# Kernel optimization log

Hardware: AMD Instinct MI355X
Metric: run time of the kernel (lower is better)

The kernel has to match this reference:

```python
import jax, jax.numpy as jnp
import numpy as np

N = 100000
E = 2000000
IN_DIM = 5
D = 32
L = 3
EPS = 1e-5


def setup_inputs() -> dict:
    key = jax.random.key(0)
    ks = jax.random.split(key, 10)
    x = jax.random.normal(ks[0], (N, IN_DIM), dtype=jnp.float32)
    edge_index = jax.random.randint(ks[1], (2, E), 0, N, dtype=jnp.int64)
    s = 1.0 / np.sqrt(D)
    w_in = jax.random.normal(ks[2], (D, IN_DIM), dtype=jnp.float32) / np.sqrt(IN_DIM)
    b_in = jnp.zeros((D,), dtype=jnp.float32)
    w_l = jax.random.normal(ks[3], (L, D, D), dtype=jnp.float32) * s  # lin_l per layer
    b_l = jnp.zeros((L, D), dtype=jnp.float32)
    w_r = jax.random.normal(ks[4], (L, D, D), dtype=jnp.float32) * s  # lin_r per layer (no bias, as in PyG SAGEConv)
    gamma = jnp.ones((D,), dtype=jnp.float32)
    beta = jnp.zeros((D,), dtype=jnp.float32)
    return {"x": x, "edge_index": edge_index, "w_in": w_in, "b_in": b_in,
            "w_l": w_l, "b_l": b_l, "w_r": w_r, "gamma": gamma, "beta": beta}


def _layernorm(h, gamma, beta):
    mu = jnp.mean(h, axis=-1, keepdims=True)
    var = jnp.mean(jnp.square(h - mu), axis=-1, keepdims=True)
    return (h - mu) * jax.lax.rsqrt(var + EPS) * gamma + beta


def reference(x, edge_index, w_in, b_in, w_l, b_l, w_r, gamma, beta):
    src = edge_index[0]
    dst = edge_index[1]
    n = x.shape[0]
    # node in-degree for mean aggregation (0-degree nodes get 0 output, like scatter_mean)
    deg = jax.ops.segment_sum(jnp.ones((src.shape[0],), dtype=x.dtype), dst, num_segments=n)
    inv_deg = (1.0 / jnp.maximum(deg, 1.0))[:, None]  # [N,1]
    h = x @ w_in.T + b_in  # [N, D]
    for i in range(w_l.shape[0]):
        msg = h[src]  # [E, D] gather
        agg = jax.ops.segment_sum(msg, dst, num_segments=n) * inv_deg  # mean aggregate
        h = agg @ w_l[i].T + b_l[i] + h @ w_r[i].T  # SAGEConv: lin_l(aggr) + lin_r(x)
        h = _layernorm(jax.nn.relu(h), gamma, beta)
    return h
```

## Files before the change

### kernel.cpp

```cpp
#include <hip/hip_runtime.h>
#include <hip/hip_bf16.h>

#define DIM 32
#define INDIM 5
#define EPB 4096
#define NBMAX 512
#define CAP 8192

__device__ __forceinline__ unsigned short f2bf(float f) {
    unsigned u = __float_as_uint(f);
    u += 0x7FFFu + ((u >> 16) & 1u);
    return (unsigned short)(u >> 16);
}
__device__ __forceinline__ float bf2f_lo(unsigned u) { return __uint_as_float(u << 16); }
__device__ __forceinline__ float bf2f_hi(unsigned u) { return __uint_as_float(u & 0xFFFF0000u); }


__global__ __launch_bounds__(256) void bucket_count_kernel(const int* __restrict__ dst,
                                                           int* __restrict__ bcnt, int e, int nb) {
    __shared__ int hist[NBMAX];
    int t = threadIdx.x;
    for (int i = t; i < nb; i += 256) hist[i] = 0;
    __syncthreads();
    int base = blockIdx.x * EPB;
    for (int k = 0; k < EPB; k += 256) {
        int i = base + k + t;
        if (i < e) atomicAdd(&hist[dst[i] >> 8], 1);
    }
    __syncthreads();
    for (int i = t; i < nb; i += 256) {
        int h = hist[i];
        if (h) atomicAdd(&bcnt[i], h);
    }
}


__global__ void bucket_scan_kernel(const int* __restrict__ bcnt, int* __restrict__ bbase,
                                   int* __restrict__ bcur, int* __restrict__ row_ptr,
                                   int nb, int n, int e) {
    __shared__ int s[512];
    int t = threadIdx.x;
    int v = (t < nb) ? bcnt[t] : 0;
    s[t] = v;
    __syncthreads();
    for (int o = 1; o < 512; o <<= 1) {
        int a = (t >= o) ? s[t - o] : 0;
        __syncthreads();
        s[t] += a;
        __syncthreads();
    }
    if (t < nb) {
        int excl = s[t] - v;
        bbase[t] = excl;
        bcur[t] = excl;
    }
    if (t == 0) {
        bbase[nb] = e;
        row_ptr[n] = e;
    }
}


__global__ __launch_bounds__(256) void bucket_fill_kernel(const int* __restrict__ src,
                                                          const int* __restrict__ dst,
                                                          int* __restrict__ bcur,
                                                          unsigned* __restrict__ packed,
                                                          int e, int nb) {
    __shared__ unsigned sw[EPB];
    __shared__ unsigned short sb[EPB];
    __shared__ int hist[NBMAX];
    __shared__ int rbase[NBMAX];
    int t = threadIdx.x;
    for (int i = t; i < nb; i += 256) hist[i] = 0;
    __syncthreads();
    int base = blockIdx.x * EPB;
    for (int k = 0; k < EPB; k += 256) {
        int i = base + k + t;
        if (i < e) {
            int s = src[i];
            int d = dst[i];
            int b = d >> 8;
            sw[k + t] = ((unsigned)s << 8) | (unsigned)(d & 255);
            sb[k + t] = (unsigned short)b;
            atomicAdd(&hist[b], 1);
        }
    }
    __syncthreads();
    for (int i = t; i < nb; i += 256) {
        int h = hist[i];
        rbase[i] = h ? atomicAdd(&bcur[i], h) : 0;
        hist[i] = 0;
    }
    __syncthreads();
    for (int k = 0; k < EPB; k += 256) {
        int i = base + k + t;
        if (i < e) {
            int b = sb[k + t];
            int r = atomicAdd(&hist[b], 1);
            packed[rbase[b] + r] = sw[k + t];
        }
    }
}


__global__ __launch_bounds__(256) void csr_build_kernel(const unsigned* __restrict__ packed,
                                                        const int* __restrict__ bbase,
                                                        int* __restrict__ row_ptr,
                                                        int* __restrict__ esrc, int n) {
    __shared__ unsigned ew[CAP];
    __shared__ int h2[256];
    __shared__ int off[256];
    int b = blockIdx.x;
    int base = bbase[b];
    int cnt = bbase[b + 1] - base;
    int t = threadIdx.x;
    h2[t] = 0;
    __syncthreads();
    bool staged = (cnt <= CAP);
    for (int i = t; i < cnt; i += 256) {
        unsigned w = packed[base + i];
        if (staged) ew[i] = w;
        atomicAdd(&h2[w & 255], 1);
    }
    __syncthreads();
    int v = h2[t];
    off[t] = v;
    __syncthreads();
    for (int o = 1; o < 256; o <<= 1) {
        int a = (t >= o) ? off[t - o] : 0;
        __syncthreads();
        off[t] += a;
        __syncthreads();
    }
    int excl = off[t] - v;
    __syncthreads();
    off[t] = excl;
    h2[t] = 0;
    __syncthreads();
    int node = b * 256 + t;
    if (node < n) row_ptr[node] = base + excl;
    for (int i = t; i < cnt; i += 256) {
        unsigned w = staged ? ew[i] : packed[base + i];
        int dl = w & 255;
        int r = atomicAdd(&h2[dl], 1);
        esrc[base + off[dl] + r] = (int)(w >> 8);
    }
}


__global__ void input_proj_kernel(const float* __restrict__ x, const float* __restrict__ w_in,
                                  const float* __restrict__ b_in,
                                  unsigned short* __restrict__ h, int n) {
    __shared__ float sw[DIM * INDIM];
    __shared__ float sb[DIM];
    int t = threadIdx.x;
    if (t < DIM * INDIM) sw[t] = w_in[t];
    if (t < DIM) sb[t] = b_in[t];
    __syncthreads();
    int idx = blockIdx.x * 256 + t;
    int node = idx >> 5;
    int d = idx & 31;
    if (node < n) {
        const float* xr = x + (size_t)node * INDIM;
        float acc = sb[d];
#pragma unroll
        for (int k = 0; k < INDIM; k++) acc = fmaf(xr[k], sw[d * INDIM + k], acc);
        h[(size_t)node * DIM + d] = f2bf(acc);
    }
}


__global__ __launch_bounds__(256) void aggregate_kernel(
    const int* __restrict__ row_ptr, const int* __restrict__ esrc,
    const unsigned short* __restrict__ h_in, float* __restrict__ agg, int n) {
    int t = threadIdx.x;
    int node = blockIdx.x * 64 + (t >> 2);
    if (node >= n) return;
    int q = t & 3;
    int rs = row_ptr[node];
    int re = row_ptr[node + 1];
    const uint4* hv = (const uint4*)h_in;

    float a0 = 0.f, a1 = 0.f, a2 = 0.f, a3 = 0.f, a4 = 0.f, a5 = 0.f, a6 = 0.f, a7 = 0.f;
    int j = rs;
    for (; j + 4 <= re; j += 4) {
        int s0 = esrc[j], s1 = esrc[j + 1], s2 = esrc[j + 2], s3 = esrc[j + 3];
        uint4 v0 = hv[(size_t)s0 * 4 + q];
        uint4 v1 = hv[(size_t)s1 * 4 + q];
        uint4 v2 = hv[(size_t)s2 * 4 + q];
        uint4 v3 = hv[(size_t)s3 * 4 + q];
        a0 += bf2f_lo(v0.x); a1 += bf2f_hi(v0.x); a2 += bf2f_lo(v0.y); a3 += bf2f_hi(v0.y);
        a4 += bf2f_lo(v0.z); a5 += bf2f_hi(v0.z); a6 += bf2f_lo(v0.w); a7 += bf2f_hi(v0.w);
        a0 += bf2f_lo(v1.x); a1 += bf2f_hi(v1.x); a2 += bf2f_lo(v1.y); a3 += bf2f_hi(v1.y);
        a4 += bf2f_lo(v1.z); a5 += bf2f_hi(v1.z); a6 += bf2f_lo(v1.w); a7 += bf2f_hi(v1.w);
        a0 += bf2f_lo(v2.x); a1 += bf2f_hi(v2.x); a2 += bf2f_lo(v2.y); a3 += bf2f_hi(v2.y);
        a4 += bf2f_lo(v2.z); a5 += bf2f_hi(v2.z); a6 += bf2f_lo(v2.w); a7 += bf2f_hi(v2.w);
        a0 += bf2f_lo(v3.x); a1 += bf2f_hi(v3.x); a2 += bf2f_lo(v3.y); a3 += bf2f_hi(v3.y);
        a4 += bf2f_lo(v3.z); a5 += bf2f_hi(v3.z); a6 += bf2f_lo(v3.w); a7 += bf2f_hi(v3.w);
    }
    for (; j < re; ++j) {
        int s = esrc[j];
        uint4 v = hv[(size_t)s * 4 + q];
        a0 += bf2f_lo(v.x); a1 += bf2f_hi(v.x); a2 += bf2f_lo(v.y); a3 += bf2f_hi(v.y);
        a4 += bf2f_lo(v.z); a5 += bf2f_hi(v.z); a6 += bf2f_lo(v.w); a7 += bf2f_hi(v.w);
    }
    float iv = 1.f / fmaxf((float)(re - rs), 1.f);
    float* ap = agg + (size_t)node * DIM + q * 8;
    float4 f0 = make_float4(a0 * iv, a1 * iv, a2 * iv, a3 * iv);
    float4 f1 = make_float4(a4 * iv, a5 * iv, a6 * iv, a7 * iv);
    *(float4*)(ap) = f0;
    *(float4*)(ap + 4) = f1;
}


template <int LAST>
__global__ __launch_bounds__(256) void combine_kernel(
    const float* __restrict__ agg, const unsigned short* __restrict__ h_in,
    unsigned short* __restrict__ h_out_bf, float* __restrict__ out_f32,
    const float* __restrict__ wl, const float* __restrict__ bl,
    const float* __restrict__ wr, const float* __restrict__ gamma,
    const float* __restrict__ beta, int n, int ngroups) {
    __shared__ float sVec[8][2][DIM];
    int t = threadIdx.x;
    int d = t & 31;
    float wlr[DIM], wrr[DIM];
    {
        const float4* p1 = (const float4*)(wl + (size_t)d * DIM);
        const float4* p2 = (const float4*)(wr + (size_t)d * DIM);
#pragma unroll
        for (int q = 0; q < 8; q++) {
            float4 a = p1[q];
            wlr[4 * q] = a.x; wlr[4 * q + 1] = a.y; wlr[4 * q + 2] = a.z; wlr[4 * q + 3] = a.w;
            float4 c = p2[q];
            wrr[4 * q] = c.x; wrr[4 * q + 1] = c.y; wrr[4 * q + 2] = c.z; wrr[4 * q + 3] = c.w;
        }
    }
    float bias = bl[d], g = gamma[d], be = beta[d];
    for (int grp = blockIdx.x; grp < ngroups; grp += gridDim.x) {
        int nb8 = grp * 8;
        __syncthreads();
        if (t < 64) {
            int nd = t >> 3, q = t & 7;
            int node = nb8 + nd;
            float4 f = make_float4(0.f, 0.f, 0.f, 0.f);
            if (node < n) f = ((const float4*)agg)[(size_t)node * 8 + q];
            *(float4*)&sVec[nd][0][q * 4] = f;
        } else if (t < 128) {
            int tt = t - 64, nd = tt >> 3, q = tt & 7;
            int node = nb8 + nd;
            uint2 v = make_uint2(0u, 0u);
            if (node < n) v = ((const uint2*)h_in)[(size_t)node * 8 + q];
            float4 f;
            f.x = bf2f_lo(v.x); f.y = bf2f_hi(v.x);
            f.z = bf2f_lo(v.y); f.w = bf2f_hi(v.y);
            *(float4*)&sVec[nd][1][q * 4] = f;
        }
        __syncthreads();
        int nd = t >> 5;
        int node = nb8 + nd;
        if (node < n) {
            float o = bias;
            const float* va = sVec[nd][0];
            const float* vs = sVec[nd][1];
#pragma unroll
            for (int q = 0; q < 8; q++) {
                float4 a = *(const float4*)&va[q * 4];
                float4 s = *(const float4*)&vs[q * 4];
                o = fmaf(a.x, wlr[4 * q], o);     o = fmaf(s.x, wrr[4 * q], o);
                o = fmaf(a.y, wlr[4 * q + 1], o); o = fmaf(s.y, wrr[4 * q + 1], o);
                o = fmaf(a.z, wlr[4 * q + 2], o); o = fmaf(s.z, wrr[4 * q + 2], o);
                o = fmaf(a.w, wlr[4 * q + 3], o); o = fmaf(s.w, wrr[4 * q + 3], o);
            }
            float out = fmaxf(o, 0.f);
            float sum = out, sq = out * out;
#pragma unroll
            for (int off = 16; off > 0; off >>= 1) {
                sum += __shfl_xor(sum, off, 32);
                sq += __shfl_xor(sq, off, 32);
            }
            float mu = sum * (1.f / 32.f);
            float var = fmaxf(sq * (1.f / 32.f) - mu * mu, 0.f);
            float r = rsqrtf(var + 1e-5f);
            float res = (out - mu) * r * g + be;
            if (LAST) out_f32[(size_t)node * DIM + d] = res;
            else      h_out_bf[(size_t)node * DIM + d] = f2bf(res);
        }
    }
}


extern "C" void kernel_launch(void* const* d_in, const int* in_sizes, int n_in,
                              void* d_out, int out_size, void* d_ws, size_t ws_size,
                              hipStream_t stream) {
    const float* x = (const float*)d_in[0];
    const int* ei = (const int*)d_in[1];
    const float* w_in = (const float*)d_in[2];
    const float* b_in = (const float*)d_in[3];
    const float* w_l = (const float*)d_in[4];
    const float* b_l = (const float*)d_in[5];
    const float* w_r = (const float*)d_in[6];
    const float* gamma = (const float*)d_in[7];
    const float* beta = (const float*)d_in[8];

    int n = in_sizes[0] / INDIM;
    int e = in_sizes[1] / 2;
    int L = in_sizes[4] / (DIM * DIM);
    const int* src = ei;
    const int* dst = ei + e;
    int nb = (n + 255) >> 8;

    char* w = (char*)d_ws;
    int* bcnt = (int*)w;               w += (size_t)NBMAX * 4;
    int* bbase = (int*)w;              w += (size_t)(NBMAX + 1) * 4;
    int* bcur = (int*)w;               w += (size_t)NBMAX * 4;
    int* row_ptr = (int*)w;            w += (size_t)(n + 1) * 4;
    int* esrc = (int*)w;               w += (size_t)e * 4;
    unsigned short* h_A = (unsigned short*)w;  w += (size_t)n * DIM * 2;
    unsigned short* h_B = (unsigned short*)w;  w += (size_t)n * DIM * 2;
    unsigned* packed = (unsigned*)h_A;
    float* aggf = (float*)d_out;

    int nbE = (e + EPB - 1) / EPB;

    hipMemsetAsync(bcnt, 0, (size_t)nb * 4, stream);
    bucket_count_kernel<<<nbE, 256, 0, stream>>>(dst, bcnt, e, nb);
    bucket_scan_kernel<<<1, 512, 0, stream>>>(bcnt, bbase, bcur, row_ptr, nb, n, e);
    bucket_fill_kernel<<<nbE, 256, 0, stream>>>(src, dst, bcur, packed, e, nb);
    csr_build_kernel<<<nb, 256, 0, stream>>>(packed, bbase, row_ptr, esrc, n);

    input_proj_kernel<<<(n * DIM + 255) / 256, 256, 0, stream>>>(x, w_in, b_in, h_A, n);

    unsigned short* bufs[2] = {h_A, h_B};
    int ngroups = (n + 7) / 8;
    int nbA = (n + 63) / 64;
    for (int i = 0; i < L; i++) {
        const unsigned short* hin = bufs[i & 1];
        unsigned short* hout = bufs[(i + 1) & 1];
        const float* wl = w_l + (size_t)i * DIM * DIM;
        const float* bl = b_l + (size_t)i * DIM;
        const float* wr = w_r + (size_t)i * DIM * DIM;
        aggregate_kernel<<<nbA, 256, 0, stream>>>(row_ptr, esrc, hin, aggf, n);
        if (i == L - 1)
            combine_kernel<1><<<1024, 256, 0, stream>>>(aggf, hin, nullptr, (float*)d_out,
                                                        wl, bl, wr, gamma, beta, n, ngroups);
        else
            combine_kernel<0><<<1024, 256, 0, stream>>>(aggf, hin, hout, nullptr,
                                                        wl, bl, wr, gamma, beta, n, ngroups);
    }
}
```

Before: 268.1 us.

## Fuse neighbor aggregation with linear combine and layernorm per layer

Merges the aggregate and combine kernels into one per-layer kernel. Each block gathers and means the neighbors for 64 nodes into shared memory, then applies lin_l/lin_r, ReLU and layernorm from that shared data. This removes the fp32 agg round trip through global memory and one launch per layer, and the gather loop is unrolled to 8 edges. The cost is higher register and LDS pressure: 64 weight registers per thread plus 16KB of shared memory, with launch bounds requesting 4 blocks per CU.

```diff
diff --git a/kernel.cpp b/kernel.cpp
--- a/kernel.cpp
+++ b/kernel.cpp
@@ -170,106 +170,109 @@
 }
 
 
-__global__ __launch_bounds__(256) void aggregate_kernel(
+template <int LAST>
+__global__ __launch_bounds__(256, 4) void layer_fused_kernel(
     const int* __restrict__ row_ptr, const int* __restrict__ esrc,
-    const unsigned short* __restrict__ h_in, float* __restrict__ agg, int n) {
-    int t = threadIdx.x;
-    int node = blockIdx.x * 64 + (t >> 2);
-    if (node >= n) return;
-    int q = t & 3;
-    int rs = row_ptr[node];
-    int re = row_ptr[node + 1];
-    const uint4* hv = (const uint4*)h_in;
-
-    float a0 = 0.f, a1 = 0.f, a2 = 0.f, a3 = 0.f, a4 = 0.f, a5 = 0.f, a6 = 0.f, a7 = 0.f;
-    int j = rs;
-    for (; j + 4 <= re; j += 4) {
-        int s0 = esrc[j], s1 = esrc[j + 1], s2 = esrc[j + 2], s3 = esrc[j + 3];
-        uint4 v0 = hv[(size_t)s0 * 4 + q];
-        uint4 v1 = hv[(size_t)s1 * 4 + q];
-        uint4 v2 = hv[(size_t)s2 * 4 + q];
-        uint4 v3 = hv[(size_t)s3 * 4 + q];
-        a0 += bf2f_lo(v0.x); a1 += bf2f_hi(v0.x); a2 += bf2f_lo(v0.y); a3 += bf2f_hi(v0.y);
-        a4 += bf2f_lo(v0.z); a5 += bf2f_hi(v0.z); a6 += bf2f_lo(v0.w); a7 += bf2f_hi(v0.w);
-        a0 += bf2f_lo(v1.x); a1 += bf2f_hi(v1.x); a2 += bf2f_lo(v1.y); a3 += bf2f_hi(v1.y);
-        a4 += bf2f_lo(v1.z); a5 += bf2f_hi(v1.z); a6 += bf2f_lo(v1.w); a7 += bf2f_hi(v1.w);
-        a0 += bf2f_lo(v2.x); a1 += bf2f_hi(v2.x); a2 += bf2f_lo(v2.y); a3 += bf2f_hi(v2.y);
-        a4 += bf2f_lo(v2.z); a5 += bf2f_hi(v2.z); a6 += bf2f_lo(v2.w); a7 += bf2f_hi(v2.w);
-        a0 += bf2f_lo(v3.x); a1 += bf2f_hi(v3.x); a2 += bf2f_lo(v3.y); a3 += bf2f_hi(v3.y);
-        a4 += bf2f_lo(v3.z); a5 += bf2f_hi(v3.z); a6 += bf2f_lo(v3.w); a7 += bf2f_hi(v3.w);
-    }
-    for (; j < re; ++j) {
-        int s = esrc[j];
-        uint4 v = hv[(size_t)s * 4 + q];
-        a0 += bf2f_lo(v.x); a1 += bf2f_hi(v.x); a2 += bf2f_lo(v.y); a3 += bf2f_hi(v.y);
-        a4 += bf2f_lo(v.z); a5 += bf2f_hi(v.z); a6 += bf2f_lo(v.w); a7 += bf2f_hi(v.w);
-    }
-    float iv = 1.f / fmaxf((float)(re - rs), 1.f);
-    float* ap = agg + (size_t)node * DIM + q * 8;
-    float4 f0 = make_float4(a0 * iv, a1 * iv, a2 * iv, a3 * iv);
-    float4 f1 = make_float4(a4 * iv, a5 * iv, a6 * iv, a7 * iv);
-    *(float4*)(ap) = f0;
-    *(float4*)(ap + 4) = f1;
-}
-
-
-template <int LAST>
-__global__ __launch_bounds__(256) void combine_kernel(
-    const float* __restrict__ agg, const unsigned short* __restrict__ h_in,
+    const unsigned short* __restrict__ h_in,
     unsigned short* __restrict__ h_out_bf, float* __restrict__ out_f32,
     const float* __restrict__ wl, const float* __restrict__ bl,
     const float* __restrict__ wr, const float* __restrict__ gamma,
-    const float* __restrict__ beta, int n, int ngroups) {
-    __shared__ float sVec[8][2][DIM];
+    const float* __restrict__ beta, int n) {
+    __shared__ float sAgg[64][DIM];
+    __shared__ float sSelf[64][DIM];
+
     int t = threadIdx.x;
     int d = t & 31;
+
     float wlr[DIM], wrr[DIM];
     {
         const float4* p1 = (const float4*)(wl + (size_t)d * DIM);
         const float4* p2 = (const float4*)(wr + (size_t)d * DIM);
 #pragma unroll
-        for (int q = 0; q < 8; q++) {
-            float4 a = p1[q];
-            wlr[4 * q] = a.x; wlr[4 * q + 1] = a.y; wlr[4 * q + 2] = a.z; wlr[4 * q + 3] = a.w;
-            float4 c = p2[q];
-            wrr[4 * q] = c.x; wrr[4 * q + 1] = c.y; wrr[4 * q + 2] = c.z; wrr[4 * q + 3] = c.w;
+        for (int qq = 0; qq < 8; qq++) {
+            float4 a = p1[qq];
+            wlr[4 * qq] = a.x; wlr[4 * qq + 1] = a.y; wlr[4 * qq + 2] = a.z; wlr[4 * qq + 3] = a.w;
+            float4 c = p2[qq];
+            wrr[4 * qq] = c.x; wrr[4 * qq + 1] = c.y; wrr[4 * qq + 2] = c.z; wrr[4 * qq + 3] = c.w;
         }
     }
     float bias = bl[d], g = gamma[d], be = beta[d];
-    for (int grp = blockIdx.x; grp < ngroups; grp += gridDim.x) {
-        int nb8 = grp * 8;
-        __syncthreads();
-        if (t < 64) {
-            int nd = t >> 3, q = t & 7;
-            int node = nb8 + nd;
-            float4 f = make_float4(0.f, 0.f, 0.f, 0.f);
-            if (node < n) f = ((const float4*)agg)[(size_t)node * 8 + q];
-            *(float4*)&sVec[nd][0][q * 4] = f;
-        } else if (t < 128) {
-            int tt = t - 64, nd = tt >> 3, q = tt & 7;
-            int node = nb8 + nd;
-            uint2 v = make_uint2(0u, 0u);
-            if (node < n) v = ((const uint2*)h_in)[(size_t)node * 8 + q];
-            float4 f;
-            f.x = bf2f_lo(v.x); f.y = bf2f_hi(v.x);
-            f.z = bf2f_lo(v.y); f.w = bf2f_hi(v.y);
-            *(float4*)&sVec[nd][1][q * 4] = f;
-        }
-        __syncthreads();
-        int nd = t >> 5;
-        int node = nb8 + nd;
-        if (node < n) {
+
+    int nd = t >> 2;
+    int q = t & 3;
+    int node = blockIdx.x * 64 + nd;
+    const uint4* hv = (const uint4*)h_in;
+
+    if (node < n) {
+        {
+            uint4 v = hv[(size_t)node * 4 + q];
+            float4 f0 = make_float4(bf2f_lo(v.x), bf2f_hi(v.x), bf2f_lo(v.y), bf2f_hi(v.y));
+            float4 f1 = make_float4(bf2f_lo(v.z), bf2f_hi(v.z), bf2f_lo(v.w), bf2f_hi(v.w));
+            *(float4*)&sSelf[nd][q * 8] = f0;
+            *(float4*)&sSelf[nd][q * 8 + 4] = f1;
+        }
+        int rs = row_ptr[node];
+        int re = row_ptr[node + 1];
+        float a0 = 0.f, a1 = 0.f, a2 = 0.f, a3 = 0.f, a4 = 0.f, a5 = 0.f, a6 = 0.f, a7 = 0.f;
+        int j = rs;
+        for (; j + 8 <= re; j += 8) {
+            int s0 = esrc[j], s1 = esrc[j + 1], s2 = esrc[j + 2], s3 = esrc[j + 3];
+            int s4 = esrc[j + 4], s5 = esrc[j + 5], s6 = esrc[j + 6], s7 = esrc[j + 7];
+            uint4 v0 = hv[(size_t)s0 * 4 + q];
+            uint4 v1 = hv[(size_t)s1 * 4 + q];
+            uint4 v2 = hv[(size_t)s2 * 4 + q];
+            uint4 v3 = hv[(size_t)s3 * 4 + q];
+            uint4 v4 = hv[(size_t)s4 * 4 + q];
+            uint4 v5 = hv[(size_t)s5 * 4 + q];
+            uint4 v6 = hv[(size_t)s6 * 4 + q];
+            uint4 v7 = hv[(size_t)s7 * 4 + q];
+            a0 += bf2f_lo(v0.x); a1 += bf2f_hi(v0.x); a2 += bf2f_lo(v0.y); a3 += bf2f_hi(v0.y);
+            a4 += bf2f_lo(v0.z); a5 += bf2f_hi(v0.z); a6 += bf2f_lo(v0.w); a7 += bf2f_hi(v0.w);
+            a0 += bf2f_lo(v1.x); a1 += bf2f_hi(v1.x); a2 += bf2f_lo(v1.y); a3 += bf2f_hi(v1.y);
+            a4 += bf2f_lo(v1.z); a5 += bf2f_hi(v1.z); a6 += bf2f_lo(v1.w); a7 += bf2f_hi(v1.w);
+            a0 += bf2f_lo(v2.x); a1 += bf2f_hi(v2.x); a2 += bf2f_lo(v2.y); a3 += bf2f_hi(v2.y);
+            a4 += bf2f_lo(v2.z); a5 += bf2f_hi(v2.z); a6 += bf2f_lo(v2.w); a7 += bf2f_hi(v2.w);
+            a0 += bf2f_lo(v3.x); a1 += bf2f_hi(v3.x); a2 += bf2f_lo(v3.y); a3 += bf2f_hi(v3.y);
+            a4 += bf2f_lo(v3.z); a5 += bf2f_hi(v3.z); a6 += bf2f_lo(v3.w); a7 += bf2f_hi(v3.w);
+            a0 += bf2f_lo(v4.x); a1 += bf2f_hi(v4.x); a2 += bf2f_lo(v4.y); a3 += bf2f_hi(v4.y);
+            a4 += bf2f_lo(v4.z); a5 += bf2f_hi(v4.z); a6 += bf2f_lo(v4.w); a7 += bf2f_hi(v4.w);
+            a0 += bf2f_lo(v5.x); a1 += bf2f_hi(v5.x); a2 += bf2f_lo(v5.y); a3 += bf2f_hi(v5.y);
+            a4 += bf2f_lo(v5.z); a5 += bf2f_hi(v5.z); a6 += bf2f_lo(v5.w); a7 += bf2f_hi(v5.w);
+            a0 += bf2f_lo(v6.x); a1 += bf2f_hi(v6.x); a2 += bf2f_lo(v6.y); a3 += bf2f_hi(v6.y);
+            a4 += bf2f_lo(v6.z); a5 += bf2f_hi(v6.z); a6 += bf2f_lo(v6.w); a7 += bf2f_hi(v6.w);
+            a0 += bf2f_lo(v7.x); a1 += bf2f_hi(v7.x); a2 += bf2f_lo(v7.y); a3 += bf2f_hi(v7.y);
+            a4 += bf2f_lo(v7.z); a5 += bf2f_hi(v7.z); a6 += bf2f_lo(v7.w); a7 += bf2f_hi(v7.w);
+        }
+        for (; j < re; ++j) {
+            int s = esrc[j];
+            uint4 v = hv[(size_t)s * 4 + q];
+            a0 += bf2f_lo(v.x); a1 += bf2f_hi(v.x); a2 += bf2f_lo(v.y); a3 += bf2f_hi(v.y);
+            a4 += bf2f_lo(v.z); a5 += bf2f_hi(v.z); a6 += bf2f_lo(v.w); a7 += bf2f_hi(v.w);
+        }
+        float iv = 1.f / fmaxf((float)(re - rs), 1.f);
+        float4 f0 = make_float4(a0 * iv, a1 * iv, a2 * iv, a3 * iv);
+        float4 f1 = make_float4(a4 * iv, a5 * iv, a6 * iv, a7 * iv);
+        *(float4*)&sAgg[nd][q * 8] = f0;
+        *(float4*)&sAgg[nd][q * 8 + 4] = f1;
+    }
+    __syncthreads();
+
+#pragma unroll
+    for (int it = 0; it < 8; ++it) {
+        int ln = it * 8 + (t >> 5);
+        int nodec = blockIdx.x * 64 + ln;
+        if (nodec < n) {
             float o = bias;
-            const float* va = sVec[nd][0];
-            const float* vs = sVec[nd][1];
-#pragma unroll
-            for (int q = 0; q < 8; q++) {
-                float4 a = *(const float4*)&va[q * 4];
-                float4 s = *(const float4*)&vs[q * 4];
-                o = fmaf(a.x, wlr[4 * q], o);     o = fmaf(s.x, wrr[4 * q], o);
-                o = fmaf(a.y, wlr[4 * q + 1], o); o = fmaf(s.y, wrr[4 * q + 1], o);
-                o = fmaf(a.z, wlr[4 * q + 2], o); o = fmaf(s.z, wrr[4 * q + 2], o);
-                o = fmaf(a.w, wlr[4 * q + 3], o); o = fmaf(s.w, wrr[4 * q + 3], o);
+            const float* va = sAgg[ln];
+            const float* vs = sSelf[ln];
+#pragma unroll
+            for (int qq = 0; qq < 8; qq++) {
+                float4 a = *(const float4*)&va[qq * 4];
+                float4 s = *(const float4*)&vs[qq * 4];
+                o = fmaf(a.x, wlr[4 * qq], o);     o = fmaf(s.x, wrr[4 * qq], o);
+                o = fmaf(a.y, wlr[4 * qq + 1], o); o = fmaf(s.y, wrr[4 * qq + 1], o);
+                o = fmaf(a.z, wlr[4 * qq + 2], o); o = fmaf(s.z, wrr[4 * qq + 2], o);
+                o = fmaf(a.w, wlr[4 * qq + 3], o); o = fmaf(s.w, wrr[4 * qq + 3], o);
             }
             float out = fmaxf(o, 0.f);
             float sum = out, sq = out * out;
@@ -282,8 +285,8 @@
             float var = fmaxf(sq * (1.f / 32.f) - mu * mu, 0.f);
             float r = rsqrtf(var + 1e-5f);
             float res = (out - mu) * r * g + be;
-            if (LAST) out_f32[(size_t)node * DIM + d] = res;
-            else      h_out_bf[(size_t)node * DIM + d] = f2bf(res);
+            if (LAST) out_f32[(size_t)nodec * DIM + d] = res;
+            else      h_out_bf[(size_t)nodec * DIM + d] = f2bf(res);
         }
     }
 }
@@ -318,7 +321,6 @@
     unsigned short* h_A = (unsigned short*)w;  w += (size_t)n * DIM * 2;
     unsigned short* h_B = (unsigned short*)w;  w += (size_t)n * DIM * 2;
     unsigned* packed = (unsigned*)h_A;
-    float* aggf = (float*)d_out;
 
     int nbE = (e + EPB - 1) / EPB;
 
@@ -331,20 +333,20 @@
     input_proj_kernel<<<(n * DIM + 255) / 256, 256, 0, stream>>>(x, w_in, b_in, h_A, n);
 
     unsigned short* bufs[2] = {h_A, h_B};
-    int ngroups = (n + 7) / 8;
-    int nbA = (n + 63) / 64;
+    int nbF = (n + 63) / 64;
     for (int i = 0; i < L; i++) {
         const unsigned short* hin = bufs[i & 1];
         unsigned short* hout = bufs[(i + 1) & 1];
         const float* wl = w_l + (size_t)i * DIM * DIM;
         const float* bl = b_l + (size_t)i * DIM;
         const float* wr = w_r + (size_t)i * DIM * DIM;
-        aggregate_kernel<<<nbA, 256, 0, stream>>>(row_ptr, esrc, hin, aggf, n);
         if (i == L - 1)
-            combine_kernel<1><<<1024, 256, 0, stream>>>(aggf, hin, nullptr, (float*)d_out,
-                                                        wl, bl, wr, gamma, beta, n, ngroups);
+            layer_fused_kernel<1><<<nbF, 256, 0, stream>>>(row_ptr, esrc, hin, nullptr,
+                                                           (float*)d_out, wl, bl, wr,
+                                                           gamma, beta, n);
         else
-            combine_kernel<0><<<1024, 256, 0, stream>>>(aggf, hin, hout, nullptr,
-                                                        wl, bl, wr, gamma, beta, n, ngroups);
-    }
-}
+            layer_fused_kernel<0><<<nbF, 256, 0, stream>>>(row_ptr, esrc, hin, hout,
+                                                           nullptr, wl, bl, wr,
+                                                           gamma, beta, n);
+    }
+}
```

Measured after the change: 252.1 us. 1.06x faster.
